# Optimization experiments

Measured on AMD Instinct MI355X. Metric: run time of the kernel, lower is better.

## Reference

```python
import jax, jax.numpy as jnp
import numpy as np

B, T, E, H = 2, 2048, 2048, 16
D = E // H  # head dim = 128
ROPE_BASE = 10000.0


def setup_inputs() -> dict:
    key = jax.random.key(0)
    ks = jax.random.split(key, 9)
    s = 1.0 / np.sqrt(E)
    return {
        "x": jax.random.normal(ks[0], (B, T, E), jnp.float32),
        "Wq": jax.random.normal(ks[1], (E, E), jnp.float32) * s,
        "bq": jax.random.normal(ks[2], (E,), jnp.float32) * s,
        "Wk": jax.random.normal(ks[3], (E, E), jnp.float32) * s,
        "bk": jax.random.normal(ks[4], (E,), jnp.float32) * s,
        "Wv": jax.random.normal(ks[5], (E, E), jnp.float32) * s,
        "bv": jax.random.normal(ks[6], (E,), jnp.float32) * s,
        "Wo": jax.random.normal(ks[7], (E, E), jnp.float32) * s,
        "bo": jax.random.normal(ks[8], (E,), jnp.float32) * s,
    }


def _rope(x):
    # x: [b, h, t, d]; positions are 1-indexed (m+1) as in the source
    t, d = x.shape[-2], x.shape[-1]
    j = jnp.arange(d // 2, dtype=x.dtype)
    thetas = ROPE_BASE ** (-2.0 * j / d)                  # [d/2]
    m = jnp.arange(1, t + 1, dtype=x.dtype)               # [t]
    ang = m[:, None] * thetas[None, :]                    # [t, d/2]
    C = jnp.concatenate([ang, ang], axis=-1)              # [t, d]
    x_rot = jnp.concatenate([-x[..., d // 2:], x[..., :d // 2]], axis=-1)
    return x * jnp.cos(C) + x_rot * jnp.sin(C)


def reference(x, Wq, bq, Wk, bk, Wv, bv, Wo, bo):
    b, t, e = x.shape
    # projections (nn.Linear: x @ W.T + b)
    def proj(W, bias):
        y = jnp.einsum('bte,fe->btf', x, W) + bias
        return y.reshape(b, t, H, D).transpose(0, 2, 1, 3)  # b h t d
    q = _rope(proj(Wq, bq))
    k = _rope(proj(Wk, bk))
    v = proj(Wv, bv)

    scale = jnp.sqrt(jnp.asarray(D, x.dtype))
    att = jnp.einsum('bhqd,bhkd->bhqk', q, k) / scale
    causal = jnp.tril(jnp.ones((t, t), bool))
    att = jnp.where(causal, att, -jnp.inf)
    att = jax.nn.softmax(att, axis=-1)
    y = jnp.einsum('bhqk,bhkd->bhqd', att, v)
    y = y.transpose(0, 2, 1, 3).reshape(b, t, e)
    y = jnp.einsum('bte,fe->btf', y, Wo) + bo
    return y
```

## Files before the change

### kernel.cpp

```cpp
#include <hip/hip_runtime.h>
#include <hip/hip_bf16.h>

typedef __bf16 bf16_t;
typedef __bf16 bf16x4 __attribute__((ext_vector_type(4)));
typedef __bf16 bf16x8 __attribute__((ext_vector_type(8)));
typedef float  f32x4  __attribute__((ext_vector_type(4)));

#define GLD_LDS16(gptr, lptr)                                                        \
    __builtin_amdgcn_global_load_lds((__attribute__((address_space(1))) void*)(gptr),\
                                     (__attribute__((address_space(3))) void*)(lptr),\
                                     16, 0, 0)

constexpr int Bc = 2, Tc = 2048, Ec = 2048, Hc = 16, Dc = 128;
constexpr int Mtok = Bc * Tc;

__device__ __forceinline__ bf16x8 cvt8(const float* p) {
    f32x4 a = *(const f32x4*)p;
    f32x4 b = *(const f32x4*)(p + 4);
    bf16x8 r;
    r[0] = (bf16_t)a[0]; r[1] = (bf16_t)a[1];
    r[2] = (bf16_t)a[2]; r[3] = (bf16_t)a[3];
    r[4] = (bf16_t)b[0]; r[5] = (bf16_t)b[1];
    r[6] = (bf16_t)b[2]; r[7] = (bf16_t)b[3];
    return r;
}

__device__ __forceinline__ float fmax_dpp16(float x) {
    int xi;
    xi = __builtin_amdgcn_mov_dpp(__builtin_bit_cast(int, x), 0xB1, 0xF, 0xF, true);
    x = fmaxf(x, __builtin_bit_cast(float, xi));
    xi = __builtin_amdgcn_mov_dpp(__builtin_bit_cast(int, x), 0x4E, 0xF, 0xF, true);
    x = fmaxf(x, __builtin_bit_cast(float, xi));
    xi = __builtin_amdgcn_mov_dpp(__builtin_bit_cast(int, x), 0x141, 0xF, 0xF, true);
    x = fmaxf(x, __builtin_bit_cast(float, xi));
    xi = __builtin_amdgcn_mov_dpp(__builtin_bit_cast(int, x), 0x140, 0xF, 0xF, true);
    x = fmaxf(x, __builtin_bit_cast(float, xi));
    return x;
}

__global__ void convert_bf16(const float* __restrict__ src, bf16_t* __restrict__ dst) {
    size_t i = ((size_t)blockIdx.x * 256 + threadIdx.x) * 8;
    *(bf16x8*)&dst[i] = cvt8(src + i);
}

__global__ void convert_w(const float* __restrict__ Wq, const float* __restrict__ Wk,
                          const float* __restrict__ Wv, const float* __restrict__ Wo,
                          bf16_t* __restrict__ w4) {
    int blk = blockIdx.x;
    int wi  = blk >> 11;
    const float* src = (wi == 0) ? Wq : (wi == 1) ? Wk : (wi == 2) ? Wv : Wo;
    bf16_t* dst = w4 + (size_t)wi * Ec * Ec;
    size_t i = ((size_t)(blk & 2047) * 256 + threadIdx.x) * 8;
    *(bf16x8*)&dst[i] = cvt8(src + i);
}

__global__ __launch_bounds__(512, 2) void gemm_qkv_z(const bf16_t* __restrict__ A,
                                                     const bf16_t* __restrict__ w3,
                                                     const float* __restrict__ bq,
                                                     const float* __restrict__ bk,
                                                     const float* __restrict__ bv,
                                                     bf16_t* __restrict__ qo,
                                                     bf16_t* __restrict__ ko,
                                                     bf16_t* __restrict__ vto) {
    __shared__ __align__(16) bf16_t ldsA[3 * 8192];
    __shared__ __align__(16) bf16_t ldsB[3 * 12288];

    const int tid  = threadIdx.x;
    const int wave = tid >> 6;
    const int lane = tid & 63;
    const int g    = lane >> 4;
    const int n16  = lane & 15;
    const int wm   = wave >> 2;
    const int wn   = wave & 3;
    const int m0   = blockIdx.x * 256;
    const int n0   = blockIdx.y * 384;
    const int K    = Ec;

    const int sr   = tid >> 2;
    const int scol = (((tid & 3) ^ ((tid >> 3) & 3)) << 3);
    const bf16_t* srcA = A  + (size_t)(m0 + sr) * K + scol;
    const bf16_t* srcB = w3 + (size_t)(n0 + sr) * K + scol;
    const int dwave = wave * 512;

    const int fsw = (n16 >> 1) & 3;

    constexpr int NT = Ec / 32;

#define STG_A2(jj, buf)                                                         \
    do { if ((jj) < NT) {                                                       \
        const bf16_t* _s = srcA + (jj) * 32;                                    \
        bf16_t* _d = &ldsA[(buf) * 8192 + dwave];                               \
        GLD_LDS16(_s, _d);                                                      \
        GLD_LDS16(_s + (size_t)128 * K, _d + 4096);                             \
    } } while (0)
#define STG_B1(jj, buf)                                                         \
    do { if ((jj) < NT) {                                                       \
        GLD_LDS16(srcB + (jj) * 32, &ldsB[(buf) * 12288 + dwave]);              \
    } } while (0)
#define STG_B2(jj, buf)                                                         \
    do { if ((jj) < NT) {                                                       \
        const bf16_t* _s = srcB + (jj) * 32;                                    \
        bf16_t* _d = &ldsB[(buf) * 12288 + dwave];                              \
        GLD_LDS16(_s + (size_t)128 * K, _d + 4096);                             \
        GLD_LDS16(_s + (size_t)256 * K, _d + 8192);                             \
    } } while (0)

    f32x4 acc[8][6] = {};
    bf16x8 af[4], af2[4], bfr[6];

    STG_A2(0, 0); STG_B1(0, 0); STG_B2(0, 0);
    STG_A2(1, 1); STG_B1(1, 1); STG_B2(1, 1);
    asm volatile("s_waitcnt vmcnt(5)" ::: "memory");
    __builtin_amdgcn_s_barrier();
    asm volatile("" ::: "memory");

    int bc = 0;
    int bi = 2;
#pragma unroll 1
    for (int j = 0; j < NT; ++j) {
        const bf16_t* la = &ldsA[bc * 8192];
        const bf16_t* lb = &ldsB[bc * 12288];

#pragma unroll
        for (int mt = 0; mt < 4; ++mt)
            af[mt] = *(const bf16x8*)&la[(wm * 128 + mt * 16 + n16) * 32 +
                                         ((g ^ fsw) << 3)];
#pragma unroll
        for (int l = 0; l < 6; ++l)
            bfr[l] = *(const bf16x8*)&lb[(wn * 96 + l * 16 + n16) * 32 +
                                         ((g ^ fsw) << 3)];
        STG_A2(j + 2, bi);
        STG_B1(j + 2, bi);
        asm volatile("s_waitcnt lgkmcnt(0)" ::: "memory");
        __builtin_amdgcn_sched_barrier(0);
        __builtin_amdgcn_s_setprio(1);
#pragma unroll
        for (int mt = 0; mt < 4; ++mt)
#pragma unroll
            for (int l = 0; l < 6; ++l)
                acc[mt][l] = __builtin_amdgcn_mfma_f32_16x16x32_bf16(
                    af[mt], bfr[l], acc[mt][l], 0, 0, 0);
        __builtin_amdgcn_s_setprio(0);
        __builtin_amdgcn_s_barrier();
        asm volatile("" ::: "memory");

#pragma unroll
        for (int mt = 0; mt < 4; ++mt)
            af2[mt] = *(const bf16x8*)&la[(wm * 128 + 64 + mt * 16 + n16) * 32 +
                                          ((g ^ fsw) << 3)];
        STG_B2(j + 2, bi);
        asm volatile("s_waitcnt lgkmcnt(0)" ::: "memory");
        __builtin_amdgcn_sched_barrier(0);
        __builtin_amdgcn_s_setprio(1);
#pragma unroll
        for (int mt = 0; mt < 4; ++mt)
#pragma unroll
            for (int l = 0; l < 6; ++l)
                acc[4 + mt][l] = __builtin_amdgcn_mfma_f32_16x16x32_bf16(
                    af2[mt], bfr[l], acc[4 + mt][l], 0, 0, 0);
        __builtin_amdgcn_s_setprio(0);

        if (j < NT - 2)      { asm volatile("s_waitcnt vmcnt(5)" ::: "memory"); }
        else if (j < NT - 1) { asm volatile("s_waitcnt vmcnt(0)" ::: "memory"); }
        __builtin_amdgcn_s_barrier();
        asm volatile("" ::: "memory");

        bc = (bc == 2) ? 0 : bc + 1;
        bi = (bi == 2) ? 0 : bi + 1;
    }
#undef STG_A2
#undef STG_B1
#undef STG_B2

#pragma unroll
    for (int l = 0; l < 6; ++l) {
        int n   = n0 + wn * 96 + l * 16 + n16;
        int mat = n >> 11;
        int nn  = n & 2047;
        const float* bp = (mat == 0) ? bq : (mat == 1) ? bk : bv;
        float bn = bp[nn];
        int h = nn >> 7, d = nn & (Dc - 1);
#pragma unroll
        for (int i = 0; i < 8; ++i) {
            int mb = m0 + wm * 128 + (i >> 2) * 64 + (i & 3) * 16 + g * 4;
            int b = mb >> 11, t = mb & (Tc - 1);
            if (mat == 2) {
                bf16x4 pk;
#pragma unroll
                for (int r = 0; r < 4; ++r) pk[r] = (bf16_t)(acc[i][l][r] + bn);
                *(bf16x4*)&vto[(((size_t)(b * Hc + h)) * Dc + d) * Tc + t] = pk;
            } else {
                bf16_t* outb = (mat == 0) ? qo : ko;
#pragma unroll
                for (int r = 0; r < 4; ++r)
                    outb[(((size_t)(b * Hc + h)) * Tc + (t + r)) * Dc + d] =
                        (bf16_t)(acc[i][l][r] + bn);
            }
        }
    }
}

__global__ __launch_bounds__(512, 2) void gemm_out_p(const bf16_t* __restrict__ A,
                                                     const bf16_t* __restrict__ W,
                                                     const float* __restrict__ bias,
                                                     float* __restrict__ out) {
    __shared__ __align__(16) bf16_t ldsA[3 * 256 * 32];
    __shared__ __align__(16) bf16_t ldsB[3 * 128 * 32];

    const int tid  = threadIdx.x;
    const int wave = tid >> 6;
    const int lane = tid & 63;
    const int g    = lane >> 4;
    const int n16  = lane & 15;
    const int wm   = wave >> 1;
    const int wn   = wave & 1;
    const int m0   = blockIdx.x * 256;
    const int n0   = blockIdx.y * 128;
    const int K    = Ec;

    const int sr   = tid >> 2;
    const int scol = (((tid & 3) ^ ((tid >> 3) & 3)) << 3);
    const bf16_t* gA0 = A + (size_t)(m0 + sr) * K + scol;
    const bf16_t* gA1 = A + (size_t)(m0 + 128 + sr) * K + scol;
    const bf16_t* gB  = W + (size_t)(n0 + sr) * K + scol;
    const int dL = wave * 512;

    const int fsw = (n16 >> 1) & 3;
    const int rAo = (wm * 64 + n16) * 32 + ((g ^ fsw) << 3);
    const int rBo = (wn * 64 + n16) * 32 + ((g ^ fsw) << 3);

    f32x4 acc[4][4] = {};

    constexpr int NT = Ec / 32;
#pragma unroll
    for (int tt = 0; tt < 2; ++tt) {
        GLD_LDS16(gA0 + tt * 32, &ldsA[tt * 8192 + dL]);
        GLD_LDS16(gA1 + tt * 32, &ldsA[tt * 8192 + 4096 + dL]);
        GLD_LDS16(gB  + tt * 32, &ldsB[tt * 4096 + dL]);
    }

    int bc = 0, bi = 2;
#pragma unroll 1
    for (int t = 0; t < NT; ++t) {
        if (t < NT - 1) { asm volatile("s_waitcnt vmcnt(3)" ::: "memory"); }
        else            { asm volatile("s_waitcnt vmcnt(0)" ::: "memory"); }
        __builtin_amdgcn_s_barrier();
        asm volatile("" ::: "memory");

        const bf16_t* la = &ldsA[bc * 8192];
        const bf16_t* lb = &ldsB[bc * 4096];
        bf16x8 af[4], bfr[4];
#pragma unroll
        for (int mt = 0; mt < 4; ++mt) af[mt] = *(const bf16x8*)&la[rAo + mt * 512];
#pragma unroll
        for (int nt = 0; nt < 4; ++nt) bfr[nt] = *(const bf16x8*)&lb[rBo + nt * 512];

        if (t + 2 < NT) {
            GLD_LDS16(gA0 + (t + 2) * 32, &ldsA[bi * 8192 + dL]);
            GLD_LDS16(gA1 + (t + 2) * 32, &ldsA[bi * 8192 + 4096 + dL]);
            GLD_LDS16(gB  + (t + 2) * 32, &ldsB[bi * 4096 + dL]);
        }

        asm volatile("s_waitcnt lgkmcnt(0)" ::: "memory");
        __builtin_amdgcn_sched_barrier(0);
        __builtin_amdgcn_s_setprio(1);
#pragma unroll
        for (int mt = 0; mt < 4; ++mt)
#pragma unroll
            for (int nt = 0; nt < 4; ++nt)
                acc[mt][nt] = __builtin_amdgcn_mfma_f32_16x16x32_bf16(
                    af[mt], bfr[nt], acc[mt][nt], 0, 0, 0);
        __builtin_amdgcn_s_setprio(0);

        bc = (bc == 2) ? 0 : bc + 1;
        bi = (bi == 2) ? 0 : bi + 1;
    }

    const int row_off = wm * 64;
    const int col_off = wn * 64;
#pragma unroll
    for (int nt = 0; nt < 4; ++nt) {
        int n = n0 + col_off + nt * 16 + n16;
        float bn = bias[n];
#pragma unroll
        for (int mt = 0; mt < 4; ++mt) {
            int mb = m0 + row_off + mt * 16 + g * 4;
#pragma unroll
            for (int r = 0; r < 4; ++r)
                out[(size_t)(mb + r) * Ec + n] = acc[mt][nt][r] + bn;
        }
    }
}

__global__ __launch_bounds__(256) void gemm_qkv(const bf16_t* __restrict__ A,
                                                const float* __restrict__ Wq,
                                                const float* __restrict__ Wk,
                                                const float* __restrict__ Wv,
                                                const float* __restrict__ bq,
                                                const float* __restrict__ bk,
                                                const float* __restrict__ bv,
                                                bf16_t* __restrict__ qo,
                                                bf16_t* __restrict__ ko,
                                                bf16_t* __restrict__ vto) {
    __shared__ __align__(16) bf16_t ldsA[128 * 32];
    __shared__ __align__(16) bf16_t ldsB[128 * 32];

    const int tid  = threadIdx.x;
    const int wave = tid >> 6;
    const int lane = tid & 63;
    const int g    = lane >> 4;
    const int n16  = lane & 15;
    const int m0   = blockIdx.x * 128;
    const int mat  = blockIdx.y >> 4;
    const int n0   = (blockIdx.y & 15) * 128;
    const int row_off = (wave >> 1) * 64;
    const int col_off = (wave & 1) * 64;
    const int K = Ec;

    const float* W    = (mat == 0) ? Wq : (mat == 1) ? Wk : Wv;
    const float* bias = (mat == 0) ? bq : (mat == 1) ? bk : bv;

    f32x4 acc[4][4] = {};

    const int r0 = tid >> 2;
    const int cc = tid & 3;
    const size_t a0 = (size_t)(m0 + r0) * K + cc * 8;
    const size_t a1 = (size_t)(m0 + r0 + 64) * K + cc * 8;
    const float* pb0 = W + (size_t)(n0 + r0) * K + cc * 8;
    const float* pb1 = W + (size_t)(n0 + r0 + 64) * K + cc * 8;

    for (int k0 = 0; k0 < K; k0 += 32) {
        bf16x8 vb0 = cvt8(pb0 + k0);
        bf16x8 vb1 = cvt8(pb1 + k0);
        __syncthreads();
        GLD_LDS16(A + a0 + k0, &ldsA[(wave * 64) * 8]);
        GLD_LDS16(A + a1 + k0, &ldsA[(256 + wave * 64) * 8]);
        *(bf16x8*)&ldsB[(size_t)tid * 8]         = vb0;
        *(bf16x8*)&ldsB[(size_t)(256 + tid) * 8] = vb1;
        __syncthreads();

        bf16x8 af[4], bfr[4];
#pragma unroll
        for (int mt = 0; mt < 4; ++mt)
            af[mt] = *(const bf16x8*)&ldsA[(row_off + mt * 16 + n16) * 32 + g * 8];
#pragma unroll
        for (int nt = 0; nt < 4; ++nt)
            bfr[nt] = *(const bf16x8*)&ldsB[(col_off + nt * 16 + n16) * 32 + g * 8];
#pragma unroll
        for (int mt = 0; mt < 4; ++mt)
#pragma unroll
            for (int nt = 0; nt < 4; ++nt)
                acc[mt][nt] = __builtin_amdgcn_mfma_f32_16x16x32_bf16(
                    af[mt], bfr[nt], acc[mt][nt], 0, 0, 0);
    }

#pragma unroll
    for (int nt = 0; nt < 4; ++nt) {
        int n = n0 + col_off + nt * 16 + n16;
        float bn = bias[n];
        int h = n >> 7, d = n & (Dc - 1);
#pragma unroll
        for (int mt = 0; mt < 4; ++mt) {
            int mb = m0 + row_off + mt * 16 + g * 4;
            int b = mb >> 11, t = mb & (Tc - 1);
            if (mat == 2) {
                bf16x4 pk;
#pragma unroll
                for (int r = 0; r < 4; ++r) pk[r] = (bf16_t)(acc[mt][nt][r] + bn);
                *(bf16x4*)&vto[(((size_t)(b * Hc + h)) * Dc + d) * Tc + t] = pk;
            } else {
                bf16_t* outb = (mat == 0) ? qo : ko;
#pragma unroll
                for (int r = 0; r < 4; ++r)
                    outb[(((size_t)(b * Hc + h)) * Tc + (t + r)) * Dc + d] =
                        (bf16_t)(acc[mt][nt][r] + bn);
            }
        }
    }
}

__global__ __launch_bounds__(256) void gemm_out(const bf16_t* __restrict__ A,
                                                const float* __restrict__ W,
                                                const float* __restrict__ bias,
                                                float* __restrict__ out,
                                                int M, int N, int K) {
    __shared__ __align__(16) bf16_t ldsA[128 * 32];
    __shared__ __align__(16) bf16_t ldsB[128 * 32];

    const int tid  = threadIdx.x;
    const int wave = tid >> 6;
    const int lane = tid & 63;
    const int g    = lane >> 4;
    const int n16  = lane & 15;
    const int m0 = blockIdx.x * 128;
    const int n0 = blockIdx.y * 128;
    const int row_off = (wave >> 1) * 64;
    const int col_off = (wave & 1) * 64;

    f32x4 acc[4][4] = {};

    const int r0 = tid >> 2;
    const int cc = tid & 3;
    const size_t a0 = (size_t)(m0 + r0) * K + cc * 8;
    const size_t a1 = (size_t)(m0 + r0 + 64) * K + cc * 8;
    const float* pb0 = W + (size_t)(n0 + r0) * K + cc * 8;
    const float* pb1 = W + (size_t)(n0 + r0 + 64) * K + cc * 8;

    for (int k0 = 0; k0 < K; k0 += 32) {
        bf16x8 vb0 = cvt8(pb0 + k0);
        bf16x8 vb1 = cvt8(pb1 + k0);
        __syncthreads();
        GLD_LDS16(A + a0 + k0, &ldsA[(wave * 64) * 8]);
        GLD_LDS16(A + a1 + k0, &ldsA[(256 + wave * 64) * 8]);
        *(bf16x8*)&ldsB[(size_t)tid * 8]         = vb0;
        *(bf16x8*)&ldsB[(size_t)(256 + tid) * 8] = vb1;
        __syncthreads();

        bf16x8 af[4], bfr[4];
#pragma unroll
        for (int mt = 0; mt < 4; ++mt)
            af[mt] = *(const bf16x8*)&ldsA[(row_off + mt * 16 + n16) * 32 + g * 8];
#pragma unroll
        for (int nt = 0; nt < 4; ++nt)
            bfr[nt] = *(const bf16x8*)&ldsB[(col_off + nt * 16 + n16) * 32 + g * 8];
#pragma unroll
        for (int mt = 0; mt < 4; ++mt)
#pragma unroll
            for (int nt = 0; nt < 4; ++nt)
                acc[mt][nt] = __builtin_amdgcn_mfma_f32_16x16x32_bf16(
                    af[mt], bfr[nt], acc[mt][nt], 0, 0, 0);
    }

#pragma unroll
    for (int nt = 0; nt < 4; ++nt) {
        int n = n0 + col_off + nt * 16 + n16;
        float bn = bias[n];
#pragma unroll
        for (int mt = 0; mt < 4; ++mt) {
            int mb = m0 + row_off + mt * 16 + g * 4;
#pragma unroll
            for (int r = 0; r < 4; ++r)
                out[(size_t)(mb + r) * N + n] = acc[mt][nt][r] + bn;
        }
    }
}

__global__ void rope_kernel(bf16_t* __restrict__ q, bf16_t* __restrict__ k) {
    int row = blockIdx.x * 4 + (threadIdx.x >> 6);
    int d   = threadIdx.x & 63;
    int t   = row & (Tc - 1);
    float theta = powf(10000.0f, -(float)d * (1.0f / 64.0f));
    float ang   = (float)(t + 1) * theta;
    float sv, cv;
    sincosf(ang, &sv, &cv);
    size_t base = (size_t)row * Dc;
    float q1 = (float)q[base + d], q2 = (float)q[base + d + 64];
    q[base + d]      = (bf16_t)(q1 * cv - q2 * sv);
    q[base + d + 64] = (bf16_t)(q2 * cv + q1 * sv);
    float k1 = (float)k[base + d], k2 = (float)k[base + d + 64];
    k[base + d]      = (bf16_t)(k1 * cv - k2 * sv);
    k[base + d + 64] = (bf16_t)(k2 * cv + k1 * sv);
}

constexpr int KP = 128 + 8;
constexpr int VP = 64 + 8;
constexpr int PP = 64 + 8;

__global__ __launch_bounds__(256) void attn_kernel(const bf16_t* __restrict__ q,
                                                   const bf16_t* __restrict__ kmat,
                                                   const bf16_t* __restrict__ vt,
                                                   bf16_t* __restrict__ out) {
    __shared__ __align__(16) bf16_t k_lds[64 * KP];
    __shared__ __align__(16) bf16_t v_lds[128 * VP];
    __shared__ __align__(16) bf16_t p_lds[4 * 16 * PP];

    const int tid  = threadIdx.x;
    const int wave = tid >> 6, lane = tid & 63;
    const int g = lane >> 4, n16 = lane & 15;
    const int pi = blockIdx.x;
    const int bh = blockIdx.y;
    const size_t base = (size_t)bh * Tc * Dc;
    const int b = bh >> 4, h = bh & 15;
    const float sc2 = 0.08838834764831845f * 1.4426950408889634f;
    bf16_t* pw = &p_lds[wave * 16 * PP];

    const int kr_key = tid >> 4, kr_c = tid & 15;
    const int vr_dd  = tid >> 3, vr_c = tid & 7;

#pragma unroll 1
    for (int half = 0; half < 2; ++half) {
        const int qt = half ? pi : 31 - pi;
        const int q0 = qt * 64;

        bf16x8 qf[4];
        {
            const bf16_t* qp = q + base + (size_t)(q0 + wave * 16 + n16) * Dc + g * 8;
#pragma unroll
            for (int kk = 0; kk < 4; ++kk) qf[kk] = *(const bf16x8*)(qp + kk * 32);
        }

        float m_run[4], l_run[4];
#pragma unroll
        for (int r = 0; r < 4; ++r) { m_run[r] = -1e30f; l_run[r] = 0.0f; }
        f32x4 o_acc[8] = {};

        bf16x8 rk[4], rv[4];
#pragma unroll
        for (int i = 0; i < 4; ++i)
            rk[i] = *(const bf16x8*)&kmat[base + (size_t)(i * 16 + kr_key) * Dc + kr_c * 8];
#pragma unroll
        for (int i = 0; i < 4; ++i)
            rv[i] = *(const bf16x8*)&vt[base + (size_t)(i * 32 + vr_dd) * Tc + vr_c * 8];

#pragma unroll 1
        for (int kt = 0; kt <= qt; ++kt) {
            const int k0 = kt * 64;
            __syncthreads();
#pragma unroll
            for (int i = 0; i < 4; ++i)
                *(bf16x8*)&k_lds[(i * 16 + kr_key) * KP + kr_c * 8] = rk[i];
#pragma unroll
            for (int i = 0; i < 4; ++i)
                *(bf16x8*)&v_lds[(i * 32 + vr_dd) * VP + vr_c * 8] = rv[i];
            __syncthreads();

            if (kt < qt) {
                const int kn = k0 + 64;
#pragma unroll
                for (int i = 0; i < 4; ++i)
                    rk[i] = *(const bf16x8*)&kmat[base + (size_t)(kn + i * 16 + kr_key) * Dc + kr_c * 8];
#pragma unroll
                for (int i = 0; i < 4; ++i)
                    rv[i] = *(const bf16x8*)&vt[base + (size_t)(i * 32 + vr_dd) * Tc + kn + vr_c * 8];
            }

            f32x4 s_acc[4];
#pragma unroll
            for (int nt = 0; nt < 4; ++nt) {
                f32x4 a = {};
                int key = nt * 16 + n16;
#pragma unroll
                for (int kk = 0; kk < 4; ++kk) {
                    bf16x8 kf = *(const bf16x8*)&k_lds[key * KP + kk * 32 + g * 8];
                    a = __builtin_amdgcn_mfma_f32_16x16x32_bf16(qf[kk], kf, a, 0, 0, 0);
                }
                s_acc[nt] = a;
            }

            if (kt == qt) {
#pragma unroll
                for (int nt = 0; nt < 4; ++nt) {
                    int key = k0 + nt * 16 + n16;
#pragma unroll
                    for (int r = 0; r < 4; ++r) {
                        int qq = q0 + wave * 16 + g * 4 + r;
                        float v = s_acc[nt][r] * sc2;
                        s_acc[nt][r] = (key <= qq) ? v : -1e30f;
                    }
                }
            } else {
#pragma unroll
                for (int nt = 0; nt < 4; ++nt)
#pragma unroll
                    for (int r = 0; r < 4; ++r) s_acc[nt][r] *= sc2;
            }

            float alpha[4];
#pragma unroll
            for (int r = 0; r < 4; ++r) {
                float rm = fmaxf(fmaxf(s_acc[0][r], s_acc[1][r]),
                                 fmaxf(s_acc[2][r], s_acc[3][r]));
                rm = fmax_dpp16(rm);
                float m_new = fmaxf(m_run[r], rm);
                alpha[r] = __builtin_amdgcn_exp2f(m_run[r] - m_new);
                m_run[r] = m_new;
                float sum = 0.0f;
#pragma unroll
                for (int nt = 0; nt < 4; ++nt) {
                    float p = __builtin_amdgcn_exp2f(s_acc[nt][r] - m_new);
                    s_acc[nt][r] = p;
                    sum += p;
                }
                l_run[r] = l_run[r] * alpha[r] + sum;
            }
#pragma unroll
            for (int dt = 0; dt < 8; ++dt)
#pragma unroll
                for (int r = 0; r < 4; ++r) o_acc[dt][r] *= alpha[r];

#pragma unroll
            for (int nt = 0; nt < 4; ++nt) {
                int key = nt * 16 + n16;
#pragma unroll
                for (int r = 0; r < 4; ++r)
                    pw[(g * 4 + r) * PP + key] = (bf16_t)s_acc[nt][r];
            }
            bf16x8 pf[2];
#pragma unroll
            for (int kk = 0; kk < 2; ++kk)
                pf[kk] = *(const bf16x8*)&pw[n16 * PP + kk * 32 + g * 8];

#pragma unroll
            for (int dt = 0; dt < 8; ++dt) {
                int dd = dt * 16 + n16;
#pragma unroll
                for (int kk = 0; kk < 2; ++kk) {
                    bf16x8 vf = *(const bf16x8*)&v_lds[dd * VP + kk * 32 + g * 8];
                    o_acc[dt] = __builtin_amdgcn_mfma_f32_16x16x32_bf16(
                        pf[kk], vf, o_acc[dt], 0, 0, 0);
                }
            }
        }

        float inv_l[4];
#pragma unroll
        for (int r = 0; r < 4; ++r) {
            float s = l_run[r];
            s += __shfl_xor(s, 1, 16);
            s += __shfl_xor(s, 2, 16);
            s += __shfl_xor(s, 4, 16);
            s += __shfl_xor(s, 8, 16);
            inv_l[r] = 1.0f / s;
        }
#pragma unroll
        for (int dt = 0; dt < 8; ++dt) {
            int d = dt * 16 + n16;
#pragma unroll
            for (int r = 0; r < 4; ++r) {
                int qq = q0 + wave * 16 + g * 4 + r;
                out[((size_t)(b * Tc + qq)) * Ec + h * Dc + d] =
                    (bf16_t)(o_acc[dt][r] * inv_l[r]);
            }
        }
    }
}

extern "C" void kernel_launch(void* const* d_in, const int* in_sizes, int n_in,
                              void* d_out, int out_size, void* d_ws, size_t ws_size,
                              hipStream_t stream) {
    const float* x  = (const float*)d_in[0];
    const float* Wq = (const float*)d_in[1];
    const float* bq = (const float*)d_in[2];
    const float* Wk = (const float*)d_in[3];
    const float* bk = (const float*)d_in[4];
    const float* Wv = (const float*)d_in[5];
    const float* bv = (const float*)d_in[6];
    const float* Wo = (const float*)d_in[7];
    const float* bo = (const float*)d_in[8];
    float* out = (float*)d_out;

    char* ws = (char*)d_ws;
    const size_t sz  = (size_t)Bc * Hc * Tc * Dc * sizeof(bf16_t);
    const size_t szW = (size_t)Ec * Ec * sizeof(bf16_t);
    bf16_t* q   = (bf16_t*)(ws);
    bf16_t* k   = (bf16_t*)(ws + sz);
    bf16_t* vt  = (bf16_t*)(ws + 2 * sz);
    bf16_t* xb  = (bf16_t*)(ws + 3 * sz);
    bf16_t* att = xb;

    if (ws_size >= 4 * sz + 4 * szW) {
        bf16_t* w4 = (bf16_t*)(ws + 4 * sz);
        convert_bf16<<<Mtok * Ec / (256 * 8), 256, 0, stream>>>(x, xb);
        convert_w<<<8192, 256, 0, stream>>>(Wq, Wk, Wv, Wo, w4);
        gemm_qkv_z<<<dim3(Mtok / 256, 16), 512, 0, stream>>>(xb, w4, bq, bk, bv,
                                                             q, k, vt);
        rope_kernel<<<Bc * Hc * Tc / 4, 256, 0, stream>>>(q, k);
        attn_kernel<<<dim3(16, Bc * Hc), 256, 0, stream>>>(q, k, vt, att);
        gemm_out_p<<<dim3(Mtok / 256, Ec / 128), 512, 0, stream>>>(
            att, w4 + 3 * (size_t)Ec * Ec, bo, out);
    } else {
        convert_bf16<<<Mtok * Ec / (256 * 8), 256, 0, stream>>>(x, xb);
        gemm_qkv<<<dim3(Mtok / 128, 48), 256, 0, stream>>>(xb, Wq, Wk, Wv,
                                                           bq, bk, bv, q, k, vt);
        rope_kernel<<<Bc * Hc * Tc / 4, 256, 0, stream>>>(q, k);
        attn_kernel<<<dim3(16, Bc * Hc), 256, 0, stream>>>(q, k, vt, att);
        gemm_out<<<dim3(Mtok / 128, Ec / 128), 256, 0, stream>>>(att, Wo, bo, out,
                                                                 Mtok, Ec, Ec);
    }
}
```

Before: 391.3 us.

## Enlarge attention query tile to 128 rows with two fragments per wave

The attention kernel now gives each block a 128-row query tile, and each wave handles 32 rows as two MFMA fragments. This replaces the earlier scheme where a block processed two 64-row tiles paired for causal load balance. Each K/V tile loaded into LDS is reused across twice as many queries, which halves LDS staging and the number of barriers per unit of work. The cost is more registers per wave (two accumulator sets), plus a launch-bounds hint asking for 2 blocks per SM. It also gives up the paired-tile load balancing, so block work now varies with qt, and the grid launch (not shown) must match the new blockIdx.x range.

```diff
diff --git a/kernel.cpp b/kernel.cpp
--- a/kernel.cpp
+++ b/kernel.cpp
@@ -466,94 +466,100 @@
 constexpr int VP = 64 + 8;
 constexpr int PP = 64 + 8;
 
-__global__ __launch_bounds__(256) void attn_kernel(const bf16_t* __restrict__ q,
-                                                   const bf16_t* __restrict__ kmat,
-                                                   const bf16_t* __restrict__ vt,
-                                                   bf16_t* __restrict__ out) {
+__global__ __launch_bounds__(256, 2) void attn_kernel(const bf16_t* __restrict__ q,
+                                                      const bf16_t* __restrict__ kmat,
+                                                      const bf16_t* __restrict__ vt,
+                                                      bf16_t* __restrict__ out) {
     __shared__ __align__(16) bf16_t k_lds[64 * KP];
     __shared__ __align__(16) bf16_t v_lds[128 * VP];
-    __shared__ __align__(16) bf16_t p_lds[4 * 16 * PP];
+    __shared__ __align__(16) bf16_t p_lds[4 * 32 * PP];
 
     const int tid  = threadIdx.x;
     const int wave = tid >> 6, lane = tid & 63;
     const int g = lane >> 4, n16 = lane & 15;
-    const int pi = blockIdx.x;
+    const int qt = 15 - blockIdx.x;
     const int bh = blockIdx.y;
+    const int q0 = qt * 128;
+    const int nkt = 2 * qt + 2;
     const size_t base = (size_t)bh * Tc * Dc;
     const int b = bh >> 4, h = bh & 15;
     const float sc2 = 0.08838834764831845f * 1.4426950408889634f;
-    bf16_t* pw = &p_lds[wave * 16 * PP];
+    bf16_t* pw = &p_lds[wave * 32 * PP];
 
     const int kr_key = tid >> 4, kr_c = tid & 15;
     const int vr_dd  = tid >> 3, vr_c = tid & 7;
 
+    bf16x8 qf[2][4];
+#pragma unroll
+    for (int mf = 0; mf < 2; ++mf) {
+        const bf16_t* qp = q + base +
+            (size_t)(q0 + wave * 32 + mf * 16 + n16) * Dc + g * 8;
+#pragma unroll
+        for (int kk = 0; kk < 4; ++kk) qf[mf][kk] = *(const bf16x8*)(qp + kk * 32);
+    }
+
+    float m_run[2][4], l_run[2][4];
+#pragma unroll
+    for (int mf = 0; mf < 2; ++mf)
+#pragma unroll
+        for (int r = 0; r < 4; ++r) { m_run[mf][r] = -1e30f; l_run[mf][r] = 0.0f; }
+    f32x4 o_acc[2][8] = {};
+
+    bf16x8 rk[4], rv[4];
+#pragma unroll
+    for (int i = 0; i < 4; ++i)
+        rk[i] = *(const bf16x8*)&kmat[base + (size_t)(i * 16 + kr_key) * Dc + kr_c * 8];
+#pragma unroll
+    for (int i = 0; i < 4; ++i)
+        rv[i] = *(const bf16x8*)&vt[base + (size_t)(i * 32 + vr_dd) * Tc + vr_c * 8];
+
 #pragma unroll 1
-    for (int half = 0; half < 2; ++half) {
-        const int qt = half ? pi : 31 - pi;
-        const int q0 = qt * 64;
-
-        bf16x8 qf[4];
-        {
-            const bf16_t* qp = q + base + (size_t)(q0 + wave * 16 + n16) * Dc + g * 8;
-#pragma unroll
-            for (int kk = 0; kk < 4; ++kk) qf[kk] = *(const bf16x8*)(qp + kk * 32);
-        }
-
-        float m_run[4], l_run[4];
-#pragma unroll
-        for (int r = 0; r < 4; ++r) { m_run[r] = -1e30f; l_run[r] = 0.0f; }
-        f32x4 o_acc[8] = {};
-
-        bf16x8 rk[4], rv[4];
+    for (int kt = 0; kt < nkt; ++kt) {
+        const int k0 = kt * 64;
+        __syncthreads();
 #pragma unroll
         for (int i = 0; i < 4; ++i)
-            rk[i] = *(const bf16x8*)&kmat[base + (size_t)(i * 16 + kr_key) * Dc + kr_c * 8];
+            *(bf16x8*)&k_lds[(i * 16 + kr_key) * KP + kr_c * 8] = rk[i];
 #pragma unroll
         for (int i = 0; i < 4; ++i)
-            rv[i] = *(const bf16x8*)&vt[base + (size_t)(i * 32 + vr_dd) * Tc + vr_c * 8];
-
-#pragma unroll 1
-        for (int kt = 0; kt <= qt; ++kt) {
-            const int k0 = kt * 64;
-            __syncthreads();
+            *(bf16x8*)&v_lds[(i * 32 + vr_dd) * VP + vr_c * 8] = rv[i];
+        __syncthreads();
+
+        if (kt + 1 < nkt) {
+            const int kn = k0 + 64;
 #pragma unroll
             for (int i = 0; i < 4; ++i)
-                *(bf16x8*)&k_lds[(i * 16 + kr_key) * KP + kr_c * 8] = rk[i];
+                rk[i] = *(const bf16x8*)&kmat[base + (size_t)(kn + i * 16 + kr_key) * Dc + kr_c * 8];
 #pragma unroll
             for (int i = 0; i < 4; ++i)
-                *(bf16x8*)&v_lds[(i * 32 + vr_dd) * VP + vr_c * 8] = rv[i];
-            __syncthreads();
-
-            if (kt < qt) {
-                const int kn = k0 + 64;
-#pragma unroll
-                for (int i = 0; i < 4; ++i)
-                    rk[i] = *(const bf16x8*)&kmat[base + (size_t)(kn + i * 16 + kr_key) * Dc + kr_c * 8];
-#pragma unroll
-                for (int i = 0; i < 4; ++i)
-                    rv[i] = *(const bf16x8*)&vt[base + (size_t)(i * 32 + vr_dd) * Tc + kn + vr_c * 8];
-            }
-
-            f32x4 s_acc[4];
-#pragma unroll
-            for (int nt = 0; nt < 4; ++nt) {
-                f32x4 a = {};
-                int key = nt * 16 + n16;
-#pragma unroll
-                for (int kk = 0; kk < 4; ++kk) {
-                    bf16x8 kf = *(const bf16x8*)&k_lds[key * KP + kk * 32 + g * 8];
-                    a = __builtin_amdgcn_mfma_f32_16x16x32_bf16(qf[kk], kf, a, 0, 0, 0);
-                }
-                s_acc[nt] = a;
-            }
-
-            if (kt == qt) {
+                rv[i] = *(const bf16x8*)&vt[base + (size_t)(i * 32 + vr_dd) * Tc + kn + vr_c * 8];
+        }
+
+        f32x4 s0[4], s1[4];
+#pragma unroll
+        for (int nt = 0; nt < 4; ++nt) {
+            f32x4 a0 = {}, a1 = {};
+            int key = nt * 16 + n16;
+#pragma unroll
+            for (int kk = 0; kk < 4; ++kk) {
+                bf16x8 kf = *(const bf16x8*)&k_lds[key * KP + kk * 32 + g * 8];
+                a0 = __builtin_amdgcn_mfma_f32_16x16x32_bf16(qf[0][kk], kf, a0, 0, 0, 0);
+                a1 = __builtin_amdgcn_mfma_f32_16x16x32_bf16(qf[1][kk], kf, a1, 0, 0, 0);
+            }
+            s0[nt] = a0; s1[nt] = a1;
+        }
+
+        const bool need_mask = (kt >= nkt - 2);
+#pragma unroll
+        for (int mf = 0; mf < 2; ++mf) {
+            f32x4* s_acc = mf ? s1 : s0;
+            if (need_mask) {
 #pragma unroll
                 for (int nt = 0; nt < 4; ++nt) {
                     int key = k0 + nt * 16 + n16;
 #pragma unroll
                     for (int r = 0; r < 4; ++r) {
-                        int qq = q0 + wave * 16 + g * 4 + r;
+                        int qq = q0 + wave * 32 + mf * 16 + g * 4 + r;
                         float v = s_acc[nt][r] * sc2;
                         s_acc[nt][r] = (key <= qq) ? v : -1e30f;
                     }
@@ -571,9 +577,9 @@
                 float rm = fmaxf(fmaxf(s_acc[0][r], s_acc[1][r]),
                                  fmaxf(s_acc[2][r], s_acc[3][r]));
                 rm = fmax_dpp16(rm);
-                float m_new = fmaxf(m_run[r], rm);
-                alpha[r] = __builtin_amdgcn_exp2f(m_run[r] - m_new);
-                m_run[r] = m_new;
+                float m_new = fmaxf(m_run[mf][r], rm);
+                alpha[r] = __builtin_amdgcn_exp2f(m_run[mf][r] - m_new);
+                m_run[mf][r] = m_new;
                 float sum = 0.0f;
 #pragma unroll
                 for (int nt = 0; nt < 4; ++nt) {
@@ -581,41 +587,49 @@
                     s_acc[nt][r] = p;
                     sum += p;
                 }
-                l_run[r] = l_run[r] * alpha[r] + sum;
+                l_run[mf][r] = l_run[mf][r] * alpha[r] + sum;
             }
 #pragma unroll
             for (int dt = 0; dt < 8; ++dt)
 #pragma unroll
-                for (int r = 0; r < 4; ++r) o_acc[dt][r] *= alpha[r];
+                for (int r = 0; r < 4; ++r) o_acc[mf][dt][r] *= alpha[r];
 
 #pragma unroll
             for (int nt = 0; nt < 4; ++nt) {
                 int key = nt * 16 + n16;
 #pragma unroll
                 for (int r = 0; r < 4; ++r)
-                    pw[(g * 4 + r) * PP + key] = (bf16_t)s_acc[nt][r];
-            }
-            bf16x8 pf[2];
+                    pw[(mf * 16 + g * 4 + r) * PP + key] = (bf16_t)s_acc[nt][r];
+            }
+        }
+
+        bf16x8 pf[2][2];
+#pragma unroll
+        for (int mf = 0; mf < 2; ++mf)
 #pragma unroll
             for (int kk = 0; kk < 2; ++kk)
-                pf[kk] = *(const bf16x8*)&pw[n16 * PP + kk * 32 + g * 8];
-
-#pragma unroll
-            for (int dt = 0; dt < 8; ++dt) {
-                int dd = dt * 16 + n16;
-#pragma unroll
-                for (int kk = 0; kk < 2; ++kk) {
-                    bf16x8 vf = *(const bf16x8*)&v_lds[dd * VP + kk * 32 + g * 8];
-                    o_acc[dt] = __builtin_amdgcn_mfma_f32_16x16x32_bf16(
-                        pf[kk], vf, o_acc[dt], 0, 0, 0);
-                }
-            }
-        }
-
+                pf[mf][kk] = *(const bf16x8*)&pw[(mf * 16 + n16) * PP + kk * 32 + g * 8];
+
+#pragma unroll
+        for (int dt = 0; dt < 8; ++dt) {
+            int dd = dt * 16 + n16;
+#pragma unroll
+            for (int kk = 0; kk < 2; ++kk) {
+                bf16x8 vf = *(const bf16x8*)&v_lds[dd * VP + kk * 32 + g * 8];
+                o_acc[0][dt] = __builtin_amdgcn_mfma_f32_16x16x32_bf16(
+                    pf[0][kk], vf, o_acc[0][dt], 0, 0, 0);
+                o_acc[1][dt] = __builtin_amdgcn_mfma_f32_16x16x32_bf16(
+                    pf[1][kk], vf, o_acc[1][dt], 0, 0, 0);
+            }
+        }
+    }
+
+#pragma unroll
+    for (int mf = 0; mf < 2; ++mf) {
         float inv_l[4];
 #pragma unroll
         for (int r = 0; r < 4; ++r) {
-            float s = l_run[r];
+            float s = l_run[mf][r];
             s += __shfl_xor(s, 1, 16);
             s += __shfl_xor(s, 2, 16);
             s += __shfl_xor(s, 4, 16);
@@ -627,9 +641,9 @@
             int d = dt * 16 + n16;
 #pragma unroll
             for (int r = 0; r < 4; ++r) {
-                int qq = q0 + wave * 16 + g * 4 + r;
+                int qq = q0 + wave * 32 + mf * 16 + g * 4 + r;
                 out[((size_t)(b * Tc + qq)) * Ec + h * Dc + d] =
-                    (bf16_t)(o_acc[dt][r] * inv_l[r]);
+                    (bf16_t)(o_acc[mf][dt][r] * inv_l[r]);
             }
         }
     }
```

Result: slower. 414.7 us (+6.0%).
